# Performance work log

Measured on AMD Instinct MI355X. Metric: run time of the kernel, lower is better.

Reference implementation:

```python
import jax, jax.numpy as jnp
import numpy as np

B, L, G, H = 16384, 4096, 30000, 256
LN_EPS = 1e-5


def setup_inputs() -> dict:
    key = jax.random.key(0)
    k0, k1, k2, k3 = jax.random.split(key, 4)
    x = jax.random.uniform(k0, (B, L), dtype=jnp.float32)          # cell x gene expression
    gene_idx = jax.random.randint(k1, (L,), 0, G)                   # irregular gene indices
    emb = jax.random.normal(k2, (G, H), dtype=jnp.float32) * 0.005  # gene embedding table
    W1 = jax.random.normal(k3, (H, H), dtype=jnp.float32) * (1.0 / np.sqrt(H))
    b1 = jnp.zeros((H,), dtype=jnp.float32)
    gamma = jnp.ones((H,), dtype=jnp.float32)
    beta = jnp.zeros((H,), dtype=jnp.float32)
    return {"x": x, "emb": emb, "W1": W1, "b1": b1, "gamma": gamma,
            "beta": beta, "gene_idx": gene_idx}


def reference(x, emb, W1, b1, gamma, beta, gene_idx):
    # OmicsEmbedder: gather gene embeddings, then weighted aggregation per cell
    feat = emb[gene_idx]                     # [L, H]  F.embedding gather
    h = x @ feat                             # [B, H]  torch.sparse.mm(x, feat)
    # extra_linear: Linear -> ReLU -> Dropout(eval: identity) -> LayerNorm
    h = jax.nn.relu(h @ W1 + b1)             # [B, H]
    mu = jnp.mean(h, axis=-1, keepdims=True)
    var = jnp.mean(jnp.square(h - mu), axis=-1, keepdims=True)
    return gamma * (h - mu) * jax.lax.rsqrt(var + LN_EPS) + beta
```

## Files before the change

kernel.cpp:

```cpp
#include <hip/hip_runtime.h>
#include <stdint.h>

#define B_DIM 16384
#define L_DIM 4096
#define H_DIM 256
#define LN_EPS 1e-5f
#define PERM4(r) ((((r) & 7) << 1) | (((r) >> 3) & 1))

typedef unsigned short u16;
typedef __attribute__((ext_vector_type(4))) float f32x4;
typedef __attribute__((ext_vector_type(8))) short short8;

__device__ __forceinline__ u16 f2bf(float f) {
  union { float f; uint32_t u; } v; v.f = f;
  uint32_t u = v.u;
  u += 0x7FFFu + ((u >> 16) & 1u);
  return (u16)(u >> 16);
}

__device__ __forceinline__ void gload_lds16(const void* g, void* l) {
  __builtin_amdgcn_global_load_lds((const __attribute__((address_space(1))) void*)g,
                                   (__attribute__((address_space(3))) void*)l, 16, 0, 0);
}

__global__ __launch_bounds__(256) void prep_frag(const float* __restrict__ src,
                                                 const int* __restrict__ idx,
                                                 u16* __restrict__ dst) {
  const int t = threadIdx.x;
  const int l = t & 63;
  const int w = t >> 6;
  const int frag = blockIdx.x * 4 + w;
  const int kstep = frag >> 4;
  const int nt = frag & 15;
  const int n = nt * 16 + (l & 15);
  const int kbase = kstep * 32 + (l >> 4) * 8;
  short8 v;
#pragma unroll
  for (int j = 0; j < 8; ++j) {
    const int k = kbase + j;
    const int g = idx ? idx[k] : k;
    v[j] = (short)f2bf(src[(size_t)g * H_DIM + n]);
  }
  *reinterpret_cast<short8*>(dst + ((size_t)frag * 64 + l) * 8) = v;
}

__global__ __launch_bounds__(256, 2) void fused(const float* __restrict__ x,
                                                const u16* __restrict__ fragB,
                                                const u16* __restrict__ fragW,
                                                const float* __restrict__ b1,
                                                const float* __restrict__ gmm,
                                                const float* __restrict__ bta,
                                                float* __restrict__ out) {
  __shared__ __align__(16) char pool[81920];
  const int t = threadIdx.x;
  const int l = t & 63;
  const int w = t >> 6;
  const int wm = w >> 1;
  const int wn = w & 1;
  const int m0 = blockIdx.x * 32;
  const float* xbase = x + (size_t)m0 * L_DIM;
  char* const bufA = pool + 65536;

#pragma unroll
  for (int i = 0; i < 2; ++i) {
    const int R = (w * 2 + i) * 4 + (l >> 4);
    const int c16 = (l & 15) ^ PERM4(R);
    gload_lds16(xbase + (size_t)R * L_DIM + c16 * 4, bufA + (w * 2 + i) * 1024);
  }
#pragma unroll
  for (int i = 0; i < 8; ++i) {
    const int j = w * 8 + i;
    gload_lds16(fragB + (size_t)j * 512 + l * 8, pool + j * 1024);
  }

  f32x4 acc[8] = {};
  const int arow = wm * 16 + (l & 15);
  const int p4 = PERM4(arow);

  for (int s = 0; s < 64; ++s) {
    asm volatile("s_waitcnt vmcnt(0)" ::: "memory");
    __builtin_amdgcn_s_barrier();
    __builtin_amdgcn_sched_barrier(0);
    if (s < 63) {
      const int nb = (s + 1) & 1;
      const u16* srcB = fragB + (size_t)(s + 1) * 32 * 512;
#pragma unroll
      for (int i = 0; i < 8; ++i) {
        const int j = w * 8 + i;
        gload_lds16(srcB + (size_t)j * 512 + l * 8, pool + nb * 32768 + j * 1024);
      }
#pragma unroll
      for (int i = 0; i < 2; ++i) {
        const int R = (w * 2 + i) * 4 + (l >> 4);
        const int c16 = (l & 15) ^ PERM4(R);
        gload_lds16(xbase + (size_t)R * L_DIM + (s + 1) * 64 + c16 * 4,
                    bufA + nb * 8192 + (w * 2 + i) * 1024);
      }
    }
    __builtin_amdgcn_sched_barrier(0);
    const char* bA = bufA + (s & 1) * 8192;
    const char* bB = pool + (s & 1) * 32768;
#pragma unroll
    for (int ks = 0; ks < 2; ++ks) {
      const int gs = ks * 8 + (l >> 4) * 2;
      const float4 a0 = *(const float4*)(bA + arow * 256 + ((gs ^ p4) * 16));
      const float4 a1 = *(const float4*)(bA + arow * 256 + (((gs + 1) ^ p4) * 16));
      short8 af;
      af[0] = (short)f2bf(a0.x); af[1] = (short)f2bf(a0.y);
      af[2] = (short)f2bf(a0.z); af[3] = (short)f2bf(a0.w);
      af[4] = (short)f2bf(a1.x); af[5] = (short)f2bf(a1.y);
      af[6] = (short)f2bf(a1.z); af[7] = (short)f2bf(a1.w);
#pragma unroll
      for (int nt = 0; nt < 8; ++nt) {
        const short8 bf = *(const short8*)(bB + (ks * 16 + wn * 8 + nt) * 1024 + l * 16);
        acc[nt] = __builtin_amdgcn_mfma_f32_16x16x32_bf16(af, bf, acc[nt], 0, 0, 0);
      }
    }
    asm volatile("s_waitcnt lgkmcnt(0)" ::: "memory");
    __builtin_amdgcn_s_barrier();
  }

#pragma unroll
  for (int i = 0; i < 8; ++i) {
    const int j = w * 8 + i;
    gload_lds16(fragW + (size_t)j * 512 + l * 8, pool + j * 1024);
  }
  const int hrow_base = wm * 16 + ((l >> 4) << 2);
#pragma unroll
  for (int rr = 0; rr < 4; ++rr) {
    const int row = hrow_base + rr;
#pragma unroll
    for (int nt = 0; nt < 8; ++nt) {
      const int col = wn * 128 + nt * 16 + (l & 15);
      const int ls = (col >> 3) ^ (row & 15);
      *(u16*)(bufA + row * 512 + ls * 16 + (col & 7) * 2) = f2bf(acc[nt][rr]);
    }
  }
  asm volatile("s_waitcnt lgkmcnt(0)" ::: "memory");
  __builtin_amdgcn_s_barrier();

  f32x4 acc2[8] = {};
  for (int kt = 0; kt < 4; ++kt) {
    asm volatile("s_waitcnt vmcnt(0)" ::: "memory");
    __builtin_amdgcn_s_barrier();
    __builtin_amdgcn_sched_barrier(0);
    if (kt < 3) {
      const u16* srcW = fragW + (size_t)(kt + 1) * 32 * 512;
#pragma unroll
      for (int i = 0; i < 8; ++i) {
        const int j = w * 8 + i;
        gload_lds16(srcW + (size_t)j * 512 + l * 8,
                    pool + ((kt + 1) & 1) * 32768 + j * 1024);
      }
    }
    __builtin_amdgcn_sched_barrier(0);
    const char* bW = pool + (kt & 1) * 32768;
#pragma unroll
    for (int ksi = 0; ksi < 2; ++ksi) {
      const int ks = kt * 2 + ksi;
      const short8 af = *(const short8*)(
          bufA + arow * 512 + (((ks * 4 + (l >> 4)) ^ (arow & 15)) * 16));
#pragma unroll
      for (int nt = 0; nt < 8; ++nt) {
        const short8 bf = *(const short8*)(bW + (ksi * 16 + wn * 8 + nt) * 1024 + l * 16);
        acc2[nt] = __builtin_amdgcn_mfma_f32_16x16x32_bf16(af, bf, acc2[nt], 0, 0, 0);
      }
    }
    asm volatile("s_waitcnt lgkmcnt(0)" ::: "memory");
    __builtin_amdgcn_s_barrier();
  }

  float bv[8];
#pragma unroll
  for (int nt = 0; nt < 8; ++nt) bv[nt] = b1[wn * 128 + nt * 16 + (l & 15)];
  float s4[4], q4[4];
#pragma unroll
  for (int rr = 0; rr < 4; ++rr) {
    float s = 0.f, q = 0.f;
#pragma unroll
    for (int nt = 0; nt < 8; ++nt) {
      const float v = fmaxf(acc2[nt][rr] + bv[nt], 0.f);
      acc2[nt][rr] = v; s += v; q += v * v;
    }
#pragma unroll
    for (int m = 1; m < 16; m <<= 1) { s += __shfl_xor(s, m); q += __shfl_xor(q, m); }
    s4[rr] = s; q4[rr] = q;
  }
  float* lnred = (float*)pool;
  if ((l & 15) == 0) {
#pragma unroll
    for (int rr = 0; rr < 4; ++rr) {
      const int row = hrow_base + rr;
      lnred[(wn * 32 + row) * 2 + 0] = s4[rr];
      lnred[(wn * 32 + row) * 2 + 1] = q4[rr];
    }
  }
  __syncthreads();
  float gg[8], bb[8];
#pragma unroll
  for (int nt = 0; nt < 8; ++nt) {
    const int col = wn * 128 + nt * 16 + (l & 15);
    gg[nt] = gmm[col]; bb[nt] = bta[col];
  }
#pragma unroll
  for (int rr = 0; rr < 4; ++rr) {
    const int row = hrow_base + rr;
    const float S = lnred[row * 2 + 0] + lnred[(32 + row) * 2 + 0];
    const float Q = lnred[row * 2 + 1] + lnred[(32 + row) * 2 + 1];
    const float mu = S * (1.0f / 256.0f);
    const float rstd = rsqrtf(Q * (1.0f / 256.0f) - mu * mu + LN_EPS);
    float* op = out + (size_t)(m0 + row) * H_DIM;
#pragma unroll
    for (int nt = 0; nt < 8; ++nt) {
      const int col = wn * 128 + nt * 16 + (l & 15);
      op[col] = gg[nt] * (acc2[nt][rr] - mu) * rstd + bb[nt];
    }
  }
}

extern "C" void kernel_launch(void* const* d_in, const int* in_sizes, int n_in,
                              void* d_out, int out_size, void* d_ws, size_t ws_size,
                              hipStream_t stream) {
  const float* x    = (const float*)d_in[0];
  const float* emb  = (const float*)d_in[1];
  const float* W1   = (const float*)d_in[2];
  const float* b1   = (const float*)d_in[3];
  const float* gmm  = (const float*)d_in[4];
  const float* bta  = (const float*)d_in[5];
  const int*   gidx = (const int*)d_in[6];
  float* out = (float*)d_out;

  char* ws = (char*)d_ws;
  u16* fragB = (u16*)ws;
  u16* fragW = (u16*)(ws + (size_t)H_DIM * L_DIM * 2);

  prep_frag<<<512, 256, 0, stream>>>(emb, gidx, fragB);
  prep_frag<<<32, 256, 0, stream>>>(W1, nullptr, fragW);
  fused<<<512, 256, 0, stream>>>(x, fragB, fragW, b1, gmm, bta, out);
}
```

Before: 104.8 us.

## Pre-convert x to bf16 once per tile and retile waves across N

The x tile is now loaded into registers, converted to bf16 once by its owning thread, and stored swizzled into LDS, which halves the A staging buffer. Before, every wave re-read fp32 A from LDS and converted it redundantly. Waves are retiled so each wave covers all 32 rows and a 64-column slice, giving 2x4 MFMA tiles per wave that reuse each B fragment twice. The second GEMM and the LayerNorm reduction are adapted to four column-wise waves. The register-staged A prefetch adds VGPR pressure and a conversion step on the critical path in exchange for less LDS traffic and less conversion work.

```diff
diff --git a/kernel.cpp b/kernel.cpp
--- a/kernel.cpp
+++ b/kernel.cpp
@@ -5,7 +5,6 @@
 #define L_DIM 4096
 #define H_DIM 256
 #define LN_EPS 1e-5f
-#define PERM4(r) ((((r) & 7) << 1) | (((r) >> 3) & 1))
 
 typedef unsigned short u16;
 typedef __attribute__((ext_vector_type(4))) float f32x4;
@@ -16,6 +15,15 @@
   uint32_t u = v.u;
   u += 0x7FFFu + ((u >> 16) & 1u);
   return (u16)(u >> 16);
+}
+
+__device__ __forceinline__ short8 cvt8(const float4& u, const float4& v) {
+  short8 o;
+  o[0] = (short)f2bf(u.x); o[1] = (short)f2bf(u.y);
+  o[2] = (short)f2bf(u.z); o[3] = (short)f2bf(u.w);
+  o[4] = (short)f2bf(v.x); o[5] = (short)f2bf(v.y);
+  o[6] = (short)f2bf(v.z); o[7] = (short)f2bf(v.w);
+  return o;
 }
 
 __device__ __forceinline__ void gload_lds16(const void* g, void* l) {
@@ -51,171 +59,185 @@
                                                 const float* __restrict__ gmm,
                                                 const float* __restrict__ bta,
                                                 float* __restrict__ out) {
-  __shared__ __align__(16) char pool[81920];
+  __shared__ __align__(16) char pool[73728];
   const int t = threadIdx.x;
   const int l = t & 63;
-  const int w = t >> 6;
-  const int wm = w >> 1;
-  const int wn = w & 1;
+  const int wv = t >> 6;
   const int m0 = blockIdx.x * 32;
-  const float* xbase = x + (size_t)m0 * L_DIM;
-  char* const bufA = pool + 65536;
-
-#pragma unroll
-  for (int i = 0; i < 2; ++i) {
-    const int R = (w * 2 + i) * 4 + (l >> 4);
-    const int c16 = (l & 15) ^ PERM4(R);
-    gload_lds16(xbase + (size_t)R * L_DIM + c16 * 4, bufA + (w * 2 + i) * 1024);
-  }
+  char* const Ab = pool + 65536;
+
+  const int sr = t >> 3;
+  const int sc = t & 7;
+  const float* xsrc = x + (size_t)(m0 + sr) * L_DIM + sc * 8;
+  const int awoff = sr * 128 + ((sc ^ (sr & 7)) << 4);
+
+  float4 aP0 = *(const float4*)(xsrc);
+  float4 aP1 = *(const float4*)(xsrc + 4);
 #pragma unroll
   for (int i = 0; i < 8; ++i) {
-    const int j = w * 8 + i;
-    gload_lds16(fragB + (size_t)j * 512 + l * 8, pool + j * 1024);
-  }
-
-  f32x4 acc[8] = {};
-  const int arow = wm * 16 + (l & 15);
-  const int p4 = PERM4(arow);
-
-  for (int s = 0; s < 64; ++s) {
-    asm volatile("s_waitcnt vmcnt(0)" ::: "memory");
-    __builtin_amdgcn_s_barrier();
-    __builtin_amdgcn_sched_barrier(0);
-    if (s < 63) {
-      const int nb = (s + 1) & 1;
-      const u16* srcB = fragB + (size_t)(s + 1) * 32 * 512;
-#pragma unroll
-      for (int i = 0; i < 8; ++i) {
-        const int j = w * 8 + i;
-        gload_lds16(srcB + (size_t)j * 512 + l * 8, pool + nb * 32768 + j * 1024);
-      }
-#pragma unroll
-      for (int i = 0; i < 2; ++i) {
-        const int R = (w * 2 + i) * 4 + (l >> 4);
-        const int c16 = (l & 15) ^ PERM4(R);
-        gload_lds16(xbase + (size_t)R * L_DIM + (s + 1) * 64 + c16 * 4,
-                    bufA + nb * 8192 + (w * 2 + i) * 1024);
-      }
-    }
-    __builtin_amdgcn_sched_barrier(0);
-    const char* bA = bufA + (s & 1) * 8192;
-    const char* bB = pool + (s & 1) * 32768;
-#pragma unroll
-    for (int ks = 0; ks < 2; ++ks) {
-      const int gs = ks * 8 + (l >> 4) * 2;
-      const float4 a0 = *(const float4*)(bA + arow * 256 + ((gs ^ p4) * 16));
-      const float4 a1 = *(const float4*)(bA + arow * 256 + (((gs + 1) ^ p4) * 16));
-      short8 af;
-      af[0] = (short)f2bf(a0.x); af[1] = (short)f2bf(a0.y);
-      af[2] = (short)f2bf(a0.z); af[3] = (short)f2bf(a0.w);
-      af[4] = (short)f2bf(a1.x); af[5] = (short)f2bf(a1.y);
-      af[6] = (short)f2bf(a1.z); af[7] = (short)f2bf(a1.w);
-#pragma unroll
-      for (int nt = 0; nt < 8; ++nt) {
-        const short8 bf = *(const short8*)(bB + (ks * 16 + wn * 8 + nt) * 1024 + l * 16);
-        acc[nt] = __builtin_amdgcn_mfma_f32_16x16x32_bf16(af, bf, acc[nt], 0, 0, 0);
-      }
-    }
-    asm volatile("s_waitcnt lgkmcnt(0)" ::: "memory");
-    __builtin_amdgcn_s_barrier();
-  }
-
-#pragma unroll
-  for (int i = 0; i < 8; ++i) {
-    const int j = w * 8 + i;
-    gload_lds16(fragW + (size_t)j * 512 + l * 8, pool + j * 1024);
-  }
-  const int hrow_base = wm * 16 + ((l >> 4) << 2);
-#pragma unroll
-  for (int rr = 0; rr < 4; ++rr) {
-    const int row = hrow_base + rr;
-#pragma unroll
-    for (int nt = 0; nt < 8; ++nt) {
-      const int col = wn * 128 + nt * 16 + (l & 15);
-      const int ls = (col >> 3) ^ (row & 15);
-      *(u16*)(bufA + row * 512 + ls * 16 + (col & 7) * 2) = f2bf(acc[nt][rr]);
-    }
-  }
+    const int j = wv * 8 + i;
+    gload_lds16(fragB + (size_t)((j >> 4) * 16 + (j & 15)) * 512 + l * 8,
+                pool + j * 1024);
+  }
+  float4 aQ0 = *(const float4*)(xsrc + 64);
+  float4 aQ1 = *(const float4*)(xsrc + 68);
+  asm volatile("s_waitcnt vmcnt(0)" ::: "memory");
+  *(short8*)(Ab + awoff) = cvt8(aP0, aP1);
   asm volatile("s_waitcnt lgkmcnt(0)" ::: "memory");
   __builtin_amdgcn_s_barrier();
 
-  f32x4 acc2[8] = {};
-  for (int kt = 0; kt < 4; ++kt) {
+  f32x4 acc[2][4] = {};
+
+  auto stage = [&](int S, const float4& WR0, const float4& WR1,
+                   float4& LD0, float4& LD1) {
     asm volatile("s_waitcnt vmcnt(0)" ::: "memory");
     __builtin_amdgcn_s_barrier();
     __builtin_amdgcn_sched_barrier(0);
-    if (kt < 3) {
-      const u16* srcW = fragW + (size_t)(kt + 1) * 32 * 512;
+    if (S < 63) {
+      const u16* srcB = fragB + (size_t)(2 * (S + 1)) * 16 * 512;
+      char* dstB = pool + ((S + 1) & 1) * 32768;
 #pragma unroll
       for (int i = 0; i < 8; ++i) {
-        const int j = w * 8 + i;
-        gload_lds16(srcW + (size_t)j * 512 + l * 8,
-                    pool + ((kt + 1) & 1) * 32768 + j * 1024);
-      }
-    }
-    __builtin_amdgcn_sched_barrier(0);
-    const char* bW = pool + (kt & 1) * 32768;
-#pragma unroll
-    for (int ksi = 0; ksi < 2; ++ksi) {
-      const int ks = kt * 2 + ksi;
-      const short8 af = *(const short8*)(
-          bufA + arow * 512 + (((ks * 4 + (l >> 4)) ^ (arow & 15)) * 16));
-#pragma unroll
-      for (int nt = 0; nt < 8; ++nt) {
-        const short8 bf = *(const short8*)(bW + (ksi * 16 + wn * 8 + nt) * 1024 + l * 16);
-        acc2[nt] = __builtin_amdgcn_mfma_f32_16x16x32_bf16(af, bf, acc2[nt], 0, 0, 0);
+        const int j = wv * 8 + i;
+        gload_lds16(srcB + (size_t)((j >> 4) * 16 + (j & 15)) * 512 + l * 8,
+                    dstB + j * 1024);
+      }
+    }
+    __builtin_amdgcn_sched_barrier(0);
+    if (S < 63)
+      *(short8*)(Ab + ((S + 1) & 1) * 4096 + awoff) = cvt8(WR0, WR1);
+    if (S < 62) {
+      const float* xn = xsrc + (S + 2) * 64;
+      LD0 = *(const float4*)(xn);
+      LD1 = *(const float4*)(xn + 4);
+    }
+    __builtin_amdgcn_sched_barrier(0);
+    const char* bB = pool + (S & 1) * 32768;
+    const char* bA = Ab + (S & 1) * 4096;
+#pragma unroll
+    for (int ks = 0; ks < 2; ++ks) {
+      short8 af[2];
+#pragma unroll
+      for (int mi = 0; mi < 2; ++mi)
+        af[mi] = *(const short8*)(bA + (mi * 16 + (l & 15)) * 128 +
+                                  (((ks * 4 + (l >> 4)) ^ (l & 7)) << 4));
+#pragma unroll
+      for (int ntl = 0; ntl < 4; ++ntl) {
+        const short8 bfv = *(const short8*)(bB + (ks * 16 + wv * 4 + ntl) * 1024 + l * 16);
+#pragma unroll
+        for (int mi = 0; mi < 2; ++mi)
+          acc[mi][ntl] = __builtin_amdgcn_mfma_f32_16x16x32_bf16(af[mi], bfv, acc[mi][ntl], 0, 0, 0);
       }
     }
     asm volatile("s_waitcnt lgkmcnt(0)" ::: "memory");
     __builtin_amdgcn_s_barrier();
-  }
-
-  float bv[8];
-#pragma unroll
-  for (int nt = 0; nt < 8; ++nt) bv[nt] = b1[wn * 128 + nt * 16 + (l & 15)];
-  float s4[4], q4[4];
-#pragma unroll
-  for (int rr = 0; rr < 4; ++rr) {
-    float s = 0.f, q = 0.f;
-#pragma unroll
-    for (int nt = 0; nt < 8; ++nt) {
-      const float v = fmaxf(acc2[nt][rr] + bv[nt], 0.f);
-      acc2[nt][rr] = v; s += v; q += v * v;
-    }
-#pragma unroll
-    for (int m = 1; m < 16; m <<= 1) { s += __shfl_xor(s, m); q += __shfl_xor(q, m); }
-    s4[rr] = s; q4[rr] = q;
-  }
-  float* lnred = (float*)pool;
-  if ((l & 15) == 0) {
+  };
+
+  for (int sp = 0; sp < 32; ++sp) {
+    stage(sp * 2,     aQ0, aQ1, aP0, aP1);
+    stage(sp * 2 + 1, aP0, aP1, aQ0, aQ1);
+  }
+
+#pragma unroll
+  for (int i = 0; i < 4; ++i) {
+    const int j = wv * 4 + i;
+    gload_lds16(fragW + (size_t)j * 512 + l * 8, pool + 16384 + j * 1024);
+  }
+#pragma unroll
+  for (int mi = 0; mi < 2; ++mi)
 #pragma unroll
     for (int rr = 0; rr < 4; ++rr) {
-      const int row = hrow_base + rr;
-      lnred[(wn * 32 + row) * 2 + 0] = s4[rr];
-      lnred[(wn * 32 + row) * 2 + 1] = q4[rr];
-    }
-  }
+      const int row = mi * 16 + (l >> 4) * 4 + rr;
+#pragma unroll
+      for (int ntl = 0; ntl < 4; ++ntl) {
+        const int col = wv * 64 + ntl * 16 + (l & 15);
+        const int ls = (col >> 3) ^ (row & 15);
+        *(u16*)(pool + row * 512 + ls * 16 + (col & 7) * 2) = f2bf(acc[mi][ntl][rr]);
+      }
+    }
+  asm volatile("s_waitcnt lgkmcnt(0)" ::: "memory");
+  __builtin_amdgcn_s_barrier();
+
+  f32x4 acc2[2][4] = {};
+  for (int kt = 0; kt < 8; ++kt) {
+    asm volatile("s_waitcnt vmcnt(0)" ::: "memory");
+    __builtin_amdgcn_s_barrier();
+    __builtin_amdgcn_sched_barrier(0);
+    if (kt < 7) {
+      const u16* srcW = fragW + (size_t)(kt + 1) * 16 * 512;
+      char* dstW = pool + 16384 + ((kt + 1) & 1) * 16384;
+#pragma unroll
+      for (int i = 0; i < 4; ++i) {
+        const int j = wv * 4 + i;
+        gload_lds16(srcW + (size_t)j * 512 + l * 8, dstW + j * 1024);
+      }
+    }
+    __builtin_amdgcn_sched_barrier(0);
+    const char* bW = pool + 16384 + (kt & 1) * 16384;
+    short8 af[2];
+#pragma unroll
+    for (int mi = 0; mi < 2; ++mi) {
+      const int row = mi * 16 + (l & 15);
+      af[mi] = *(const short8*)(pool + row * 512 +
+                                (((kt * 4 + (l >> 4)) ^ (row & 15)) << 4));
+    }
+#pragma unroll
+    for (int ntl = 0; ntl < 4; ++ntl) {
+      const short8 bfv = *(const short8*)(bW + (wv * 4 + ntl) * 1024 + l * 16);
+#pragma unroll
+      for (int mi = 0; mi < 2; ++mi)
+        acc2[mi][ntl] = __builtin_amdgcn_mfma_f32_16x16x32_bf16(af[mi], bfv, acc2[mi][ntl], 0, 0, 0);
+    }
+    asm volatile("s_waitcnt lgkmcnt(0)" ::: "memory");
+    __builtin_amdgcn_s_barrier();
+  }
+
+  float bv[4], gg[4], bb[4];
+#pragma unroll
+  for (int ntl = 0; ntl < 4; ++ntl) {
+    const int col = wv * 64 + ntl * 16 + (l & 15);
+    bv[ntl] = b1[col]; gg[ntl] = gmm[col]; bb[ntl] = bta[col];
+  }
+  float* lnred = (float*)(pool + 49152);
+#pragma unroll
+  for (int mi = 0; mi < 2; ++mi)
+#pragma unroll
+    for (int rr = 0; rr < 4; ++rr) {
+      float s = 0.f, q = 0.f;
+#pragma unroll
+      for (int ntl = 0; ntl < 4; ++ntl) {
+        const float v = fmaxf(acc2[mi][ntl][rr] + bv[ntl], 0.f);
+        acc2[mi][ntl][rr] = v; s += v; q += v * v;
+      }
+#pragma unroll
+      for (int m = 1; m < 16; m <<= 1) { s += __shfl_xor(s, m); q += __shfl_xor(q, m); }
+      if ((l & 15) == 0) {
+        const int row = mi * 16 + (l >> 4) * 4 + rr;
+        lnred[(wv * 32 + row) * 2 + 0] = s;
+        lnred[(wv * 32 + row) * 2 + 1] = q;
+      }
+    }
   __syncthreads();
-  float gg[8], bb[8];
-#pragma unroll
-  for (int nt = 0; nt < 8; ++nt) {
-    const int col = wn * 128 + nt * 16 + (l & 15);
-    gg[nt] = gmm[col]; bb[nt] = bta[col];
-  }
-#pragma unroll
-  for (int rr = 0; rr < 4; ++rr) {
-    const int row = hrow_base + rr;
-    const float S = lnred[row * 2 + 0] + lnred[(32 + row) * 2 + 0];
-    const float Q = lnred[row * 2 + 1] + lnred[(32 + row) * 2 + 1];
-    const float mu = S * (1.0f / 256.0f);
-    const float rstd = rsqrtf(Q * (1.0f / 256.0f) - mu * mu + LN_EPS);
-    float* op = out + (size_t)(m0 + row) * H_DIM;
-#pragma unroll
-    for (int nt = 0; nt < 8; ++nt) {
-      const int col = wn * 128 + nt * 16 + (l & 15);
-      op[col] = gg[nt] * (acc2[nt][rr] - mu) * rstd + bb[nt];
-    }
-  }
+#pragma unroll
+  for (int mi = 0; mi < 2; ++mi)
+#pragma unroll
+    for (int rr = 0; rr < 4; ++rr) {
+      const int row = mi * 16 + (l >> 4) * 4 + rr;
+      float S = 0.f, Q = 0.f;
+#pragma unroll
+      for (int w2 = 0; w2 < 4; ++w2) {
+        S += lnred[(w2 * 32 + row) * 2 + 0];
+        Q += lnred[(w2 * 32 + row) * 2 + 1];
+      }
+      const float mu = S * (1.0f / 256.0f);
+      const float rstd = rsqrtf(Q * (1.0f / 256.0f) - mu * mu + LN_EPS);
+      float* op = out + (size_t)(m0 + row) * H_DIM;
+#pragma unroll
+      for (int ntl = 0; ntl < 4; ++ntl) {
+        const int col = wv * 64 + ntl * 16 + (l & 15);
+        op[col] = gg[ntl] * (acc2[mi][ntl][rr] - mu) * rstd + bb[ntl];
+      }
+    }
 }
 
 extern "C" void kernel_launch(void* const* d_in, const int* in_sizes, int n_in,
```

Result: slower. 108.9 us (+3.9%).
